# Kernel tuning notes

Measured on AMD Instinct MI355X. Metric: run time of the kernel, lower is better.

Reference implementation:

```python
import jax, jax.numpy as jnp
import numpy as np

IN_CH = 32
OUT_CH = 32
M1, M2 = 32, 32
BS, H, W = 8, 256, 256


def setup_inputs() -> dict:
    key = jax.random.key(0)
    kx, kk = jax.random.split(key)
    x = jax.random.normal(kx, (BS, IN_CH, H, W), dtype=jnp.float32)
    # reset_parameters: randn * (1/(in_ch*out_ch)) + 1
    scale = 1.0 / (IN_CH * OUT_CH)
    kernel = jax.random.normal(kk, (2, 1, OUT_CH, M1, M2, 2), dtype=jnp.float32) * scale + 1.0
    r = jnp.float32(1.0)
    return {"x": x, "kernel": kernel, "r": r}


def reference(x, kernel, r):
    # view_as_complex: last dim of 2 -> complex, shape [2, 1, C, M1, M2]
    kc = (kernel[..., 0] + 1j * kernel[..., 1]).astype(jnp.complex64)
    # elementwise complex power kernel**r
    kc = jnp.power(kc, r)

    # forward 2D real FFT over spatial dims (ortho norm)
    x_ft = jnp.fft.rfftn(x, axes=(-2, -1), norm="ortho")  # [bs, C, H, W//2+1]
    Hf, Wr = x_ft.shape[-2], x_ft.shape[-1]
    n1 = min(Hf // 2, M1)
    n2 = min(Wr, M2)

    def mix(block, k):
        # fft over channel dim (-3), multiply by complex kernel, ifft back
        b = jnp.fft.fft(block, axis=-3, norm="ortho")
        b = b * k[..., :n1, :n2]
        return jnp.fft.ifft(b, axis=-3, norm="ortho")

    pos = mix(x_ft[..., :n1, :n2], kc[0])          # low positive freqs
    neg = mix(x_ft[..., Hf - n1:, :n2], kc[1])     # low negative freqs

    out_ft = jnp.zeros((x.shape[0], OUT_CH, Hf, Wr), dtype=jnp.complex64)
    out_ft = out_ft.at[..., :n1, :n2].set(pos)
    out_ft = out_ft.at[..., Hf - n1:, :n2].set(neg)

    # inverse real FFT back to spatial domain
    return jnp.fft.irfftn(out_ft, s=(x.shape[-2], x.shape[-1]), axes=(-2, -1), norm="ortho")
```

## Files before the change

### kernel.cpp

```cpp
#include <hip/hip_runtime.h>
#include <math.h>


#define TWO_PI 6.28318530717958647692f

__global__ __launch_bounds__(256) void kP(const float* __restrict__ kin,
                                          const float* __restrict__ rp,
                                          float2* __restrict__ kp) {
  const int i = blockIdx.x * 256 + threadIdx.x;
  const float r = rp[0];
  const float kr = kin[2 * i], ki = kin[2 * i + 1];
  const float m2 = fmaf(kr, kr, ki * ki);
  float2 o = make_float2(0.f, 0.f);
  if (m2 > 0.f) {
    const float lm = 0.5f * logf(m2);
    const float ang = atan2f(ki, kr);
    const float mag = expf(r * lm);
    float s, c;
    sincosf(r * ang, &s, &c);
    o = make_float2(mag * c, mag * s);
  }
  kp[i] = o;
}

__global__ __launch_bounds__(256) void kA(const float* __restrict__ x,
                                          float2* __restrict__ z1) {
  __shared__ float xs[8192];
  const int tid = threadIdx.x;
  const long row0 = (long)blockIdx.x * 32;
  const float* xg = x + row0 * 256;
  {
    const int rot = (4 * tid) & 31;
    float* col = xs + tid * 32;
#pragma unroll
    for (int r = 0; r < 32; ++r) col[(r + rot) & 31] = xg[r * 256 + tid];
  }
  __syncthreads();
  for (int i = tid; i < 127 * 32; i += 256) {
    const int xi = 1 + (i >> 5), r = i & 31;
    const int ai = (xi << 5) + ((r + 4 * xi) & 31);
    const int bi = ((256 - xi) << 5) + ((r - 4 * xi) & 31);
    const float a = xs[ai], b = xs[bi];
    xs[ai] = a + b;
    xs[bi] = a - b;
  }
  __syncthreads();
  const int w = tid & 31;
  const int r0 = (tid >> 5) << 2;
  int uo[8];
#pragma unroll
  for (int j = 0; j < 8; ++j) uo[j] = ((r0 + 4 * j) & 31) << 2;
  const float sgn = (w & 1) ? -1.f : 1.f;
  const float4 x0 = *(const float4*)(xs + r0);
  const float4 x128 = *(const float4*)(xs + (128 << 5) + r0);
  float Cr0 = fmaf(sgn, x128.x, x0.x), Cr1 = fmaf(sgn, x128.y, x0.y);
  float Cr2 = fmaf(sgn, x128.z, x0.z), Cr3 = fmaf(sgn, x128.w, x0.w);
  float Ci0 = 0, Ci1 = 0, Ci2 = 0, Ci3 = 0;
  float s1, c1;
  sincosf(TWO_PI * (float)w / 256.0f, &s1, &c1);
  float pc = c1, ps = s1;
  const char* const xsb = (const char*)xs;
#define KA_BODY(UPTR, VPTR)                                        \
  {                                                                \
    const float4 u = *(const float4*)(UPTR);                       \
    const float4 v = *(const float4*)(VPTR);                       \
    Cr0 = fmaf(u.x, pc, Cr0); Ci0 = fmaf(-v.x, ps, Ci0);           \
    Cr1 = fmaf(u.y, pc, Cr1); Ci1 = fmaf(-v.y, ps, Ci1);           \
    Cr2 = fmaf(u.z, pc, Cr2); Ci2 = fmaf(-v.z, ps, Ci2);           \
    Cr3 = fmaf(u.w, pc, Cr3); Ci3 = fmaf(-v.w, ps, Ci3);           \
    const float tn = fmaf(pc, c1, -ps * s1);                       \
    ps = fmaf(pc, s1, ps * c1);                                    \
    pc = tn;                                                       \
  }
  {
    const char* ub = xsb;
    const char* vb = xsb + 249 * 128;
#pragma unroll
    for (int j = 1; j < 8; ++j)
      KA_BODY(ub + j * 128 + uo[j], vb + (7 - j) * 128 + uo[8 - j])
  }
  for (int xb = 8; xb <= 120; xb += 8) {
    const char* ub = xsb + xb * 128;
    const char* vb = xsb + (249 - xb) * 128;
#pragma unroll
    for (int j = 0; j < 8; ++j)
      KA_BODY(ub + j * 128 + uo[j], vb + (7 - j) * 128 + uo[(8 - j) & 7])
  }
#undef KA_BODY
  float2* o = z1 + (row0 + r0) * 32 + w;
  o[0]  = make_float2(Cr0, Ci0);
  o[32] = make_float2(Cr1, Ci1);
  o[64] = make_float2(Cr2, Ci2);
  o[96] = make_float2(Cr3, Ci3);
}

__global__ __launch_bounds__(256) void kB(const float2* __restrict__ z1,
                                          float2* __restrict__ z2p) {
  __shared__ float2 zs[128 * 32];
  const int bc = blockIdx.x >> 1, yh = blockIdx.x & 1;
  const float2* src = z1 + (long)bc * 8192 + yh * 4096;
  for (int i = threadIdx.x; i < 4096; i += 256) zs[i] = src[i];
  __syncthreads();
  const int t = threadIdx.x >> 2, wq = threadIdx.x & 3;
  const int h = (t < 32) ? t : (192 + t);
  float sr, cr;
  sincosf(-TWO_PI * (float)h / 256.0f, &sr, &cr);
  float pc = (yh && (t & 1)) ? -1.f : 1.f, ps = 0.f;
  float ar[8], ai[8];
#pragma unroll
  for (int k = 0; k < 8; ++k) { ar[k] = 0.f; ai[k] = 0.f; }
  const float* zb = (const float*)zs + wq * 16;
#pragma unroll 2
  for (int y = 0; y < 128; ++y) {
    const float4* zf = (const float4*)(zb + y * 64);
#pragma unroll
    for (int k = 0; k < 4; ++k) {
      const float4 q = zf[k];
      ar[2 * k]     = fmaf(q.x, pc, fmaf(-q.y, ps, ar[2 * k]));
      ai[2 * k]     = fmaf(q.x, ps, fmaf( q.y, pc, ai[2 * k]));
      ar[2 * k + 1] = fmaf(q.z, pc, fmaf(-q.w, ps, ar[2 * k + 1]));
      ai[2 * k + 1] = fmaf(q.z, ps, fmaf( q.w, pc, ai[2 * k + 1]));
    }
    const float tn = fmaf(pc, cr, -ps * sr);
    ps = fmaf(pc, sr, ps * cr);
    pc = tn;
  }
  float4* dst = (float4*)(z2p + (long)yh * 524288 + (long)bc * 2048 + t * 32 + wq * 8);
#pragma unroll
  for (int k = 0; k < 4; ++k)
    dst[k] = make_float4(ar[2 * k], ai[2 * k], ar[2 * k + 1], ai[2 * k + 1]);
}

__global__ __launch_bounds__(256) void kC(const float2* __restrict__ z2a,
                                          const float2* __restrict__ z2b,
                                          const float2* __restrict__ kp,
                                          float2* __restrict__ g) {
  __shared__ float2 z2s[16 * 33];
  __shared__ float2 fk[16 * 33];
  __shared__ float2 tw[32];
  const int tid = threadIdx.x;
  if (tid < 32) {
    float s, c;
    sincosf(-TWO_PI * (float)tid / 32.0f, &s, &c);
    tw[tid] = make_float2(c, s);
  }
  const int m0 = blockIdx.x * 16;
  const int b = m0 >> 11;
  const int twi = m0 & 2047;
  const int t = twi >> 5;
  const int w0 = twi & 31;
  const int s_ = t >> 5, tm = t & 31;
  for (int i = tid; i < 512; i += 256) {
    const int ci = i >> 4, wj = i & 15;
    const long idx = ((long)(b * 32 + ci)) * 2048 + t * 32 + w0 + wj;
    const float2 va = z2a[idx], vb = z2b[idx];
    z2s[wj * 33 + ci] = make_float2(va.x + vb.x, va.y + vb.y);
  }
  __syncthreads();
  const int m = tid & 15;
  const int p = tid >> 4;
  const int cf0 = 2 * p, cf1 = 2 * p + 1;
  {
    float f0r = 0, f0i = 0, f1r = 0, f1i = 0;
    int i0 = 0, i1 = 0;
#pragma unroll 8
    for (int ci = 0; ci < 32; ++ci) {
      const float2 z = z2s[m * 33 + ci];
      const float2 t0 = tw[i0]; i0 = (i0 + cf0) & 31;
      const float2 t1 = tw[i1]; i1 = (i1 + cf1) & 31;
      f0r = fmaf(z.x, t0.x, fmaf(-z.y, t0.y, f0r));
      f0i = fmaf(z.x, t0.y, fmaf( z.y, t0.x, f0i));
      f1r = fmaf(z.x, t1.x, fmaf(-z.y, t1.y, f1r));
      f1i = fmaf(z.x, t1.y, fmaf( z.y, t1.x, f1i));
    }
    const float2 k0 = kp[((s_ * 32 + cf0) * 32 + tm) * 32 + w0 + m];
    const float2 k1 = kp[((s_ * 32 + cf1) * 32 + tm) * 32 + w0 + m];
    fk[m * 33 + cf0] = make_float2(f0r * k0.x - f0i * k0.y, f0r * k0.y + f0i * k0.x);
    fk[m * 33 + cf1] = make_float2(f1r * k1.x - f1i * k1.y, f1r * k1.y + f1i * k1.x);
  }
  __syncthreads();
  {
    float g0r = 0, g0i = 0, g1r = 0, g1i = 0;
    int i0 = 0, i1 = 0;
    const int co0 = 2 * p, co1 = 2 * p + 1;
#pragma unroll 8
    for (int cf = 0; cf < 32; ++cf) {
      const float2 f = fk[m * 33 + cf];
      const float2 t0 = tw[i0]; i0 = (i0 + co0) & 31;
      const float2 t1 = tw[i1]; i1 = (i1 + co1) & 31;
      g0r = fmaf(f.x, t0.x, fmaf( f.y, t0.y, g0r));
      g0i = fmaf(f.y, t0.x, fmaf(-f.x, t0.y, g0i));
      g1r = fmaf(f.x, t1.x, fmaf( f.y, t1.y, g1r));
      g1i = fmaf(f.y, t1.x, fmaf(-f.x, t1.y, g1i));
    }
    const float SC = 1.0f / 8192.0f;
    g[((long)(b * 32 + co0)) * 2048 + t * 32 + w0 + m] = make_float2(g0r * SC, g0i * SC);
    g[((long)(b * 32 + co1)) * 2048 + t * 32 + w0 + m] = make_float2(g1r * SC, g1i * SC);
  }
}

__global__ __launch_bounds__(256) void kD(const float2* __restrict__ g,
                                          float2* __restrict__ tb) {
  __shared__ float2 gs[64 * 32];
  const int bc = blockIdx.x >> 1, yh = blockIdx.x & 1;
  const float2* src = g + (long)bc * 2048;
  for (int i = threadIdx.x; i < 2048; i += 256) gs[i] = src[i];
  __syncthreads();
  const int yl = threadIdx.x >> 1, wh = threadIdx.x & 1;
  const int y = yh * 128 + yl;
  float s1, c1;
  sincosf(TWO_PI * (float)y / 256.0f, &s1, &c1);
  float Tr[16], Ti[16];
#pragma unroll
  for (int k = 0; k < 16; ++k) { Tr[k] = 0.f; Ti[k] = 0.f; }
  float pc = 1.f, ps = 0.f;
  const float* gb = (const float*)gs + wh * 32;
  for (int t = 0; t < 64; ++t) {
    if (t == 32) {
      float s2, c2;
      sincosf(TWO_PI * (float)((224 * y) & 255) / 256.0f, &s2, &c2);
      pc = c2; ps = s2;
    }
    const float4* gf = (const float4*)(gb + t * 64);
#pragma unroll
    for (int k = 0; k < 8; ++k) {
      const float4 q = gf[k];
      Tr[2 * k]     = fmaf(q.x, pc, fmaf(-q.y, ps, Tr[2 * k]));
      Ti[2 * k]     = fmaf(q.x, ps, fmaf( q.y, pc, Ti[2 * k]));
      Tr[2 * k + 1] = fmaf(q.z, pc, fmaf(-q.w, ps, Tr[2 * k + 1]));
      Ti[2 * k + 1] = fmaf(q.z, ps, fmaf( q.w, pc, Ti[2 * k + 1]));
    }
    const float tn = fmaf(pc, c1, -ps * s1);
    ps = fmaf(pc, s1, ps * c1);
    pc = tn;
  }
  float4* dst = (float4*)(tb + (long)bc * 8192 + y * 32 + wh * 16);
#pragma unroll
  for (int k = 0; k < 8; ++k)
    dst[k] = make_float4(Tr[2 * k], Ti[2 * k], Tr[2 * k + 1], Ti[2 * k + 1]);
}

__global__ __launch_bounds__(256) void kE(const float2* __restrict__ tb,
                                          float* __restrict__ out) {
  __shared__ float2 tst[32 * 34];
  const long row0 = (long)blockIdx.x * 32;
  const int tid = threadIdx.x;
  for (int i = tid; i < 1024; i += 256) {
    const int w = i & 31, r = i >> 5;
    const float2 v = tb[(row0 + r) * 32 + w];
    const float sc = w ? (2.0f / 256.0f) : (1.0f / 256.0f);
    tst[w * 34 + r] = make_float2(v.x * sc, v.y * sc);
  }
  __syncthreads();
  const int xq = tid & 31;
  const int rh = tid >> 5;
  float sb, cb;
  sincosf(TWO_PI * (float)xq / 256.0f, &sb, &cb);
  const float RT = 0.70710678118654752440f;
  const float stc1 = RT * (cb - sb), sts1 = RT * (cb + sb);
  const float stc[4] = {cb, stc1, -sb, -sts1};
  const float sts[4] = {sb, sts1, cb, stc1};
  float C[4][4], S[4][4];
#pragma unroll
  for (int m = 0; m < 4; ++m)
#pragma unroll
    for (int j = 0; j < 4; ++j) { C[m][j] = 0.f; S[m][j] = 0.f; }
  float pc[4] = {1.f, 1.f, 1.f, 1.f}, ps[4] = {0.f, 0.f, 0.f, 0.f};
  const float* tbse = (const float*)tst + rh * 8;
#pragma unroll 2
  for (int w = 0; w < 32; ++w) {
    const float4 q0 = *(const float4*)(tbse + w * 68);
    const float4 q1 = *(const float4*)(tbse + w * 68 + 4);
#pragma unroll
    for (int m = 0; m < 4; ++m) {
      C[m][0] = fmaf(q0.x, pc[m], C[m][0]);
      S[m][0] = fmaf(q0.y, ps[m], S[m][0]);
      C[m][1] = fmaf(q0.z, pc[m], C[m][1]);
      S[m][1] = fmaf(q0.w, ps[m], S[m][1]);
      C[m][2] = fmaf(q1.x, pc[m], C[m][2]);
      S[m][2] = fmaf(q1.y, ps[m], S[m][2]);
      C[m][3] = fmaf(q1.z, pc[m], C[m][3]);
      S[m][3] = fmaf(q1.w, ps[m], S[m][3]);
      const float tn = fmaf(pc[m], stc[m], -ps[m] * sts[m]);
      ps[m] = fmaf(pc[m], sts[m], ps[m] * stc[m]);
      pc[m] = tn;
    }
  }
#pragma unroll
  for (int m = 0; m < 4; ++m) {
    const int xx = xq + 32 * m;
#pragma unroll
    for (int j = 0; j < 4; ++j) {
      const long row = row0 + rh * 4 + j;
      out[row * 256 + xx] = C[m][j] - S[m][j];
      out[row * 256 + ((256 - xx) & 255)] = C[m][j] + S[m][j];
    }
  }
  if (tid < 32) {
    float ae = 0.f, ao = 0.f;
#pragma unroll
    for (int k = 0; k < 16; ++k) {
      ae += tst[(2 * k) * 34 + tid].x;
      ao += tst[(2 * k + 1) * 34 + tid].x;
    }
    out[(row0 + tid) * 256 + 128] = ae - ao;
  }
}

extern "C" void kernel_launch(void* const* d_in, const int* in_sizes, int n_in,
                              void* d_out, int out_size, void* d_ws, size_t ws_size,
                              hipStream_t stream) {
  const float* x = (const float*)d_in[0];
  const float* kin = (const float*)d_in[1];
  const float* rp = (const float*)d_in[2];
  float* out = (float*)d_out;
  char* ws = (char*)d_ws;

  float2* z1  = (float2*)(ws);
  float2* z2a = (float2*)(ws + (16ull << 20));
  float2* kp  = (float2*)(ws + (24ull << 20));
  float2* g   = (float2*)(ws);
  float2* tb  = (float2*)(ws + (4ull << 20));

  kP<<<256, 256, 0, stream>>>(kin, rp, kp);
  kA<<<2048, 256, 0, stream>>>(x, z1);
  kB<<<512, 256, 0, stream>>>(z1, z2a);
  kC<<<1024, 256, 0, stream>>>(z2a, z2a + 524288, kp, g);
  kD<<<512, 256, 0, stream>>>(g, tb);
  kE<<<2048, 256, 0, stream>>>(tb, out);
}
```

Before: 211.1 us.

## Fuse inverse column DFT and row irfft kernels, vectorize kA smem transpose

Merges kD and kE into one kernel. Each block computes a 32-row slice of the y-direction inverse DFT into shared memory, then runs the x-direction real inverse transform on that slice, so the tb intermediate never goes through global memory and one launch is removed. Each block now reloads the full 2048-element g slab, which is 8x redundant global reads, and kD's work per thread shrinks. kA's global-to-shared transpose also changes to coalesced loads with float4 swizzled shared stores instead of scalar rotated stores.

New measurement: 210.3 us. Within noise of the previous version (-0.4%).

```diff
diff --git a/kernel.cpp b/kernel.cpp
--- a/kernel.cpp
+++ b/kernel.cpp
@@ -30,10 +30,15 @@
   const long row0 = (long)blockIdx.x * 32;
   const float* xg = x + row0 * 256;
   {
-    const int rot = (4 * tid) & 31;
-    float* col = xs + tid * 32;
-#pragma unroll
-    for (int r = 0; r < 32; ++r) col[(r + rot) & 31] = xg[r * 256 + tid];
+    const int xl = tid & 31, rq = tid >> 5;
+    const float* xgr = xg + rq * 4 * 256 + xl;
+#pragma unroll
+    for (int cb = 0; cb < 8; ++cb) {
+      const int xc = xl + 32 * cb;
+      const float4 v = make_float4(xgr[32 * cb], xgr[32 * cb + 256],
+                                   xgr[32 * cb + 512], xgr[32 * cb + 768]);
+      *(float4*)(xs + xc * 32 + 4 * ((rq + xc) & 7)) = v;
+    }
   }
   __syncthreads();
   for (int i = tid; i < 127 * 32; i += 256) {
@@ -199,111 +204,108 @@
   }
 }
 
-__global__ __launch_bounds__(256) void kD(const float2* __restrict__ g,
-                                          float2* __restrict__ tb) {
-  __shared__ float2 gs[64 * 32];
-  const int bc = blockIdx.x >> 1, yh = blockIdx.x & 1;
+__global__ __launch_bounds__(256) void kDE(const float2* __restrict__ g,
+                                           float* __restrict__ out) {
+  __shared__ float2 gs[2048];
+  __shared__ float2 tst[32 * 34];
+  const int tid = threadIdx.x;
+  const int bc = blockIdx.x >> 3, yq = blockIdx.x & 7;
   const float2* src = g + (long)bc * 2048;
-  for (int i = threadIdx.x; i < 2048; i += 256) gs[i] = src[i];
-  __syncthreads();
-  const int yl = threadIdx.x >> 1, wh = threadIdx.x & 1;
-  const int y = yh * 128 + yl;
-  float s1, c1;
-  sincosf(TWO_PI * (float)y / 256.0f, &s1, &c1);
-  float Tr[16], Ti[16];
-#pragma unroll
-  for (int k = 0; k < 16; ++k) { Tr[k] = 0.f; Ti[k] = 0.f; }
-  float pc = 1.f, ps = 0.f;
-  const float* gb = (const float*)gs + wh * 32;
-  for (int t = 0; t < 64; ++t) {
-    if (t == 32) {
-      float s2, c2;
-      sincosf(TWO_PI * (float)((224 * y) & 255) / 256.0f, &s2, &c2);
-      pc = c2; ps = s2;
-    }
-    const float4* gf = (const float4*)(gb + t * 64);
-#pragma unroll
-    for (int k = 0; k < 8; ++k) {
-      const float4 q = gf[k];
-      Tr[2 * k]     = fmaf(q.x, pc, fmaf(-q.y, ps, Tr[2 * k]));
-      Ti[2 * k]     = fmaf(q.x, ps, fmaf( q.y, pc, Ti[2 * k]));
-      Tr[2 * k + 1] = fmaf(q.z, pc, fmaf(-q.w, ps, Tr[2 * k + 1]));
-      Ti[2 * k + 1] = fmaf(q.z, ps, fmaf( q.w, pc, Ti[2 * k + 1]));
-    }
-    const float tn = fmaf(pc, c1, -ps * s1);
-    ps = fmaf(pc, s1, ps * c1);
-    pc = tn;
-  }
-  float4* dst = (float4*)(tb + (long)bc * 8192 + y * 32 + wh * 16);
-#pragma unroll
-  for (int k = 0; k < 8; ++k)
-    dst[k] = make_float4(Tr[2 * k], Ti[2 * k], Tr[2 * k + 1], Ti[2 * k + 1]);
-}
-
-__global__ __launch_bounds__(256) void kE(const float2* __restrict__ tb,
-                                          float* __restrict__ out) {
-  __shared__ float2 tst[32 * 34];
-  const long row0 = (long)blockIdx.x * 32;
-  const int tid = threadIdx.x;
-  for (int i = tid; i < 1024; i += 256) {
-    const int w = i & 31, r = i >> 5;
-    const float2 v = tb[(row0 + r) * 32 + w];
-    const float sc = w ? (2.0f / 256.0f) : (1.0f / 256.0f);
-    tst[w * 34 + r] = make_float2(v.x * sc, v.y * sc);
-  }
-  __syncthreads();
-  const int xq = tid & 31;
-  const int rh = tid >> 5;
-  float sb, cb;
-  sincosf(TWO_PI * (float)xq / 256.0f, &sb, &cb);
-  const float RT = 0.70710678118654752440f;
-  const float stc1 = RT * (cb - sb), sts1 = RT * (cb + sb);
-  const float stc[4] = {cb, stc1, -sb, -sts1};
-  const float sts[4] = {sb, sts1, cb, stc1};
-  float C[4][4], S[4][4];
-#pragma unroll
-  for (int m = 0; m < 4; ++m)
-#pragma unroll
-    for (int j = 0; j < 4; ++j) { C[m][j] = 0.f; S[m][j] = 0.f; }
-  float pc[4] = {1.f, 1.f, 1.f, 1.f}, ps[4] = {0.f, 0.f, 0.f, 0.f};
-  const float* tbse = (const float*)tst + rh * 8;
+  for (int i = tid; i < 2048; i += 256) gs[i] = src[i];
+  __syncthreads();
+  {
+    const int y5 = tid >> 3, wq = tid & 7;
+    const int y = yq * 32 + y5;
+    float s1, c1;
+    sincosf(TWO_PI * (float)y / 256.0f, &s1, &c1);
+    float Tr[4], Ti[4];
+#pragma unroll
+    for (int k = 0; k < 4; ++k) { Tr[k] = 0.f; Ti[k] = 0.f; }
+    float pc = 1.f, ps = 0.f;
+    const float* gb = (const float*)gs + wq * 8;
+    for (int t = 0; t < 64; ++t) {
+      if (t == 32) {
+        float s2, c2;
+        sincosf(TWO_PI * (float)((224 * y) & 255) / 256.0f, &s2, &c2);
+        pc = c2; ps = s2;
+      }
+      const float4* gf = (const float4*)(gb + t * 64);
+      const float4 qa = gf[0], qb = gf[1];
+      Tr[0] = fmaf(qa.x, pc, fmaf(-qa.y, ps, Tr[0]));
+      Ti[0] = fmaf(qa.x, ps, fmaf( qa.y, pc, Ti[0]));
+      Tr[1] = fmaf(qa.z, pc, fmaf(-qa.w, ps, Tr[1]));
+      Ti[1] = fmaf(qa.z, ps, fmaf( qa.w, pc, Ti[1]));
+      Tr[2] = fmaf(qb.x, pc, fmaf(-qb.y, ps, Tr[2]));
+      Ti[2] = fmaf(qb.x, ps, fmaf( qb.y, pc, Ti[2]));
+      Tr[3] = fmaf(qb.z, pc, fmaf(-qb.w, ps, Tr[3]));
+      Ti[3] = fmaf(qb.z, ps, fmaf( qb.w, pc, Ti[3]));
+      const float tn = fmaf(pc, c1, -ps * s1);
+      ps = fmaf(pc, s1, ps * c1);
+      pc = tn;
+    }
+#pragma unroll
+    for (int k = 0; k < 4; ++k) {
+      const int w = wq * 4 + k;
+      const float sc = w ? (2.0f / 256.0f) : (1.0f / 256.0f);
+      tst[w * 34 + y5] = make_float2(Tr[k] * sc, Ti[k] * sc);
+    }
+  }
+  __syncthreads();
+  {
+    const int xq = tid & 31;
+    const int rh = tid >> 5;
+    float sb, cb;
+    sincosf(TWO_PI * (float)xq / 256.0f, &sb, &cb);
+    const float RT = 0.70710678118654752440f;
+    const float stc1 = RT * (cb - sb), sts1 = RT * (cb + sb);
+    const float stc[4] = {cb, stc1, -sb, -sts1};
+    const float sts[4] = {sb, sts1, cb, stc1};
+    float C[4][4], S[4][4];
+#pragma unroll
+    for (int m = 0; m < 4; ++m)
+#pragma unroll
+      for (int j = 0; j < 4; ++j) { C[m][j] = 0.f; S[m][j] = 0.f; }
+    float pc[4] = {1.f, 1.f, 1.f, 1.f}, ps[4] = {0.f, 0.f, 0.f, 0.f};
+    const float* tbse = (const float*)tst + rh * 8;
 #pragma unroll 2
-  for (int w = 0; w < 32; ++w) {
-    const float4 q0 = *(const float4*)(tbse + w * 68);
-    const float4 q1 = *(const float4*)(tbse + w * 68 + 4);
+    for (int w = 0; w < 32; ++w) {
+      const float4 q0 = *(const float4*)(tbse + w * 68);
+      const float4 q1 = *(const float4*)(tbse + w * 68 + 4);
+#pragma unroll
+      for (int m = 0; m < 4; ++m) {
+        C[m][0] = fmaf(q0.x, pc[m], C[m][0]);
+        S[m][0] = fmaf(q0.y, ps[m], S[m][0]);
+        C[m][1] = fmaf(q0.z, pc[m], C[m][1]);
+        S[m][1] = fmaf(q0.w, ps[m], S[m][1]);
+        C[m][2] = fmaf(q1.x, pc[m], C[m][2]);
+        S[m][2] = fmaf(q1.y, ps[m], S[m][2]);
+        C[m][3] = fmaf(q1.z, pc[m], C[m][3]);
+        S[m][3] = fmaf(q1.w, ps[m], S[m][3]);
+        const float tn = fmaf(pc[m], stc[m], -ps[m] * sts[m]);
+        ps[m] = fmaf(pc[m], sts[m], ps[m] * stc[m]);
+        pc[m] = tn;
+      }
+    }
+    const long rbase = (long)bc * 256 + yq * 32;
 #pragma unroll
     for (int m = 0; m < 4; ++m) {
-      C[m][0] = fmaf(q0.x, pc[m], C[m][0]);
-      S[m][0] = fmaf(q0.y, ps[m], S[m][0]);
-      C[m][1] = fmaf(q0.z, pc[m], C[m][1]);
-      S[m][1] = fmaf(q0.w, ps[m], S[m][1]);
-      C[m][2] = fmaf(q1.x, pc[m], C[m][2]);
-      S[m][2] = fmaf(q1.y, ps[m], S[m][2]);
-      C[m][3] = fmaf(q1.z, pc[m], C[m][3]);
-      S[m][3] = fmaf(q1.w, ps[m], S[m][3]);
-      const float tn = fmaf(pc[m], stc[m], -ps[m] * sts[m]);
-      ps[m] = fmaf(pc[m], sts[m], ps[m] * stc[m]);
-      pc[m] = tn;
-    }
-  }
-#pragma unroll
-  for (int m = 0; m < 4; ++m) {
-    const int xx = xq + 32 * m;
-#pragma unroll
-    for (int j = 0; j < 4; ++j) {
-      const long row = row0 + rh * 4 + j;
-      out[row * 256 + xx] = C[m][j] - S[m][j];
-      out[row * 256 + ((256 - xx) & 255)] = C[m][j] + S[m][j];
-    }
-  }
-  if (tid < 32) {
-    float ae = 0.f, ao = 0.f;
-#pragma unroll
-    for (int k = 0; k < 16; ++k) {
-      ae += tst[(2 * k) * 34 + tid].x;
-      ao += tst[(2 * k + 1) * 34 + tid].x;
-    }
-    out[(row0 + tid) * 256 + 128] = ae - ao;
+      const int xx = xq + 32 * m;
+#pragma unroll
+      for (int j = 0; j < 4; ++j) {
+        const long row = rbase + rh * 4 + j;
+        out[row * 256 + xx] = C[m][j] - S[m][j];
+        out[row * 256 + ((256 - xx) & 255)] = C[m][j] + S[m][j];
+      }
+    }
+    if (tid < 32) {
+      float ae = 0.f, ao = 0.f;
+#pragma unroll
+      for (int k = 0; k < 16; ++k) {
+        ae += tst[(2 * k) * 34 + tid].x;
+        ao += tst[(2 * k + 1) * 34 + tid].x;
+      }
+      out[(rbase + tid) * 256 + 128] = ae - ao;
+    }
   }
 }
 
@@ -320,12 +322,10 @@
   float2* z2a = (float2*)(ws + (16ull << 20));
   float2* kp  = (float2*)(ws + (24ull << 20));
   float2* g   = (float2*)(ws);
-  float2* tb  = (float2*)(ws + (4ull << 20));
 
   kP<<<256, 256, 0, stream>>>(kin, rp, kp);
   kA<<<2048, 256, 0, stream>>>(x, z1);
   kB<<<512, 256, 0, stream>>>(z1, z2a);
   kC<<<1024, 256, 0, stream>>>(z2a, z2a + 524288, kp, g);
-  kD<<<512, 256, 0, stream>>>(g, tb);
-  kE<<<2048, 256, 0, stream>>>(tb, out);
-}
+  kDE<<<2048, 256, 0, stream>>>(g, out);
+}
```
